# Kernel tuning notes

Hardware: AMD Instinct MI355X
Metric: run time of the kernel (lower is better)

The kernel has to match this reference:

```python
import jax, jax.numpy as jnp
import numpy as np

DIM = 1024
NH = 16        # query heads
NKV = 4        # kv heads
HD = 64        # head dim
GROUPS = NH // NKV
SPATIAL = 16
NZ = SPATIAL * SPATIAL  # 256 latent tokens with 2D structure
SOFT_CAP = 50.0
SCALE = HD ** -0.5
EPS = 1e-6


def rope_2d_cos_sin(nz, hd, spatial, dtype):
    # 2D RoPE: first half of head_dim encodes row position, second half column.
    pos = jnp.arange(nz)
    row = (pos // spatial).astype(jnp.float32)
    col = (pos % spatial).astype(jnp.float32)
    quarter = hd // 4
    inv_freq = 1.0 / (10000.0 ** (jnp.arange(quarter, dtype=jnp.float32) / quarter))
    f_row = row[:, None] * inv_freq[None, :]   # (nz, hd/4)
    f_col = col[:, None] * inv_freq[None, :]   # (nz, hd/4)
    emb = jnp.concatenate([f_row, f_col], axis=-1)      # (nz, hd/2)
    emb = jnp.concatenate([emb, emb], axis=-1)          # (nz, hd)
    return jnp.cos(emb).astype(dtype), jnp.sin(emb).astype(dtype)


def rotate_half(x):
    x1, x2 = jnp.split(x, 2, axis=-1)
    return jnp.concatenate([-x2, x1], axis=-1)


def apply_rotary(x, cos, sin):
    return x * cos + rotate_half(x) * sin


def rms_norm(x, w):
    # RMSNorm over head_dim with learned per-dim scale (QKNorm)
    return x * jax.lax.rsqrt(jnp.mean(x * x, axis=-1, keepdims=True) + EPS) * w


def setup_inputs() -> dict:
    key = jax.random.key(0)
    ks = jax.random.split(key, 7)
    B, T, S = 4, 16, 264
    x = jax.random.normal(ks[0], (B, T, S, DIM), dtype=jnp.float32)
    wq = jax.random.normal(ks[1], (NH * HD, DIM), dtype=jnp.float32) * 0.02
    wk = jax.random.normal(ks[2], (NKV * HD, DIM), dtype=jnp.float32) * 0.02
    wv = jax.random.normal(ks[3], (NKV * HD, DIM), dtype=jnp.float32) * 0.02
    wo = jax.random.normal(ks[4], (DIM, NH * HD), dtype=jnp.float32) * 0.02
    q_norm_w = jnp.ones((HD,), dtype=jnp.float32)
    k_norm_w = jnp.ones((HD,), dtype=jnp.float32)
    return {"x": x, "wq": wq, "wk": wk, "wv": wv, "wo": wo,
            "q_norm_w": q_norm_w, "k_norm_w": k_norm_w}


def reference(x, wq, wk, wv, wo, q_norm_w, k_norm_w):
    B, T, S, D = x.shape
    xf = x.reshape(B * T, S, D)
    # projections (torch Linear: y = x @ W.T)
    q = (xf @ wq.T).reshape(B * T, S, NH, HD).transpose(0, 2, 1, 3)   # (BT,NH,S,HD)
    k = (xf @ wk.T).reshape(B * T, S, NKV, HD).transpose(0, 2, 1, 3)  # (BT,NKV,S,HD)
    v = (xf @ wv.T).reshape(B * T, S, NKV, HD).transpose(0, 2, 1, 3)
    # QKNorm
    q = rms_norm(q, q_norm_w)
    k = rms_norm(k, k_norm_w)
    # partial 2D RoPE on latent tokens only
    cos, sin = rope_2d_cos_sin(NZ, HD, SPATIAL, q.dtype)
    cos = cos[None, None]  # (1,1,NZ,HD)
    sin = sin[None, None]
    q = jnp.concatenate([apply_rotary(q[:, :, :NZ], cos, sin), q[:, :, NZ:]], axis=2)
    k = jnp.concatenate([apply_rotary(k[:, :, :NZ], cos, sin), k[:, :, NZ:]], axis=2)
    # GQA: expand kv heads (repeat_interleave == jnp.repeat)
    k = jnp.repeat(k, GROUPS, axis=1)
    v = jnp.repeat(v, GROUPS, axis=1)
    # attention with soft cap
    attn = jnp.einsum("bhqd,bhkd->bhqk", q, k) * SCALE
    attn = SOFT_CAP * jnp.tanh(attn / SOFT_CAP)
    attn = jax.nn.softmax(attn, axis=-1)
    out = jnp.einsum("bhqk,bhkd->bhqd", attn, v)
    out = out.transpose(0, 2, 1, 3).reshape(B * T, S, NH * HD)
    out = out @ wo.T
    return out.reshape(B, T, S, D)
```

## Files before the change

kernel.cpp:

```cpp
#include <hip/hip_runtime.h>

typedef __bf16 bf16;
typedef __bf16 bf16x8 __attribute__((ext_vector_type(8)));
typedef float  f32x4  __attribute__((ext_vector_type(4)));
typedef float  f32x16 __attribute__((ext_vector_type(16)));
typedef unsigned int u32;

#define DIM   1024
#define NH    16
#define NKV   4
#define HD    64
#define SLEN  264
#define BTOT  64
#define MROWS (BTOT * SLEN)
#define NQKV  1536
#define NZ    256
#define VPAD  288

__device__ __forceinline__ void gl_lds16(const bf16* g, bf16* l) {
    __builtin_amdgcn_global_load_lds((__attribute__((address_space(1))) void*)(g),
                                     (__attribute__((address_space(3))) void*)(l),
                                     16, 0, 0);
}

__global__ void cvt_f32_bf16(const float* __restrict__ src, bf16* __restrict__ dst, int n) {
    int i = (blockIdx.x * 256 + threadIdx.x) * 4;
    if (i < n) {
        float4 v = *(const float4*)(src + i);
        dst[i + 0] = (bf16)v.x; dst[i + 1] = (bf16)v.y;
        dst[i + 2] = (bf16)v.z; dst[i + 3] = (bf16)v.w;
    }
}

__global__ void prep_misc(const float* __restrict__ wq, const float* __restrict__ wk,
                          const float* __restrict__ wv, const float* __restrict__ wo,
                          bf16* __restrict__ wcat, bf16* __restrict__ wobf,
                          float2* __restrict__ ctab) {
    int b = blockIdx.x, tid = threadIdx.x;
    if (b < 1536) {
        int i = (b * 256 + tid) * 4;
        const float* src; int off;
        if (i < 1024 * 1024)      { src = wq; off = i; }
        else if (i < 1280 * 1024) { src = wk; off = i - 1024 * 1024; }
        else                      { src = wv; off = i - 1280 * 1024; }
        float4 v = *(const float4*)(src + off);
        wcat[i + 0] = (bf16)v.x; wcat[i + 1] = (bf16)v.y;
        wcat[i + 2] = (bf16)v.z; wcat[i + 3] = (bf16)v.w;
    } else if (b < 2560) {
        int i = ((b - 1536) * 256 + tid) * 4;
        float4 v = *(const float4*)(wo + i);
        wobf[i + 0] = (bf16)v.x; wobf[i + 1] = (bf16)v.y;
        wobf[i + 2] = (bf16)v.z; wobf[i + 3] = (bf16)v.w;
    } else {
        int i = (b - 2560) * 256 + tid;
        int s = i >> 5, d = i & 31;
        const float LN1 = 0.5756462732485115f;
        float pos = (d < 16) ? (float)(s >> 4) : (float)(s & 15);
        float ang = pos * expf(-(float)(d & 15) * LN1);
        float sn, cs; sincosf(ang, &sn, &cs);
        ctab[i] = make_float2(cs, sn);
    }
}

__device__ __forceinline__ int xcd_swizzle(int orig, int nwg) {
    int q = nwg >> 3, r = nwg & 7;
    int xcd = orig & 7, lid = orig >> 3;
    return (xcd < r ? xcd * (q + 1) : r * (q + 1) + (xcd - r) * q) + lid;
}

#define GATE2  asm volatile("s_waitcnt vmcnt(2)" ::: "memory")
#define NOGATE do {} while (0)

#define STAGE(DST, G, H, KT) do {                                              \
    gl_lds16((G) + (size_t)((H) * 128 + rs0) * DIM + (KT) * 64 + cs0 * 8,      \
             (DST) + wid * 512);                                               \
    gl_lds16((G) + (size_t)((H) * 128 + 64 + rs0) * DIM + (KT) * 64 + cs0 * 8, \
             (DST) + 4096 + wid * 512);                                        \
} while (0)

#define PHASE(Ad, Bd, AA, KS, STAGE_STMT, GATE_STMT) do {                      \
    bf16x8 af_[4], bf_[4];                                                     \
    _Pragma("unroll")                                                          \
    for (int i_ = 0; i_ < 4; i_++) {                                           \
        af_[i_] = *(const bf16x8*)((Ad) + aRdBase + i_ * 1024 + xorv[KS]);     \
        bf_[i_] = *(const bf16x8*)((Bd) + bRdBase + i_ * 1024 + xorv[KS]);     \
    }                                                                          \
    STAGE_STMT;                                                                \
    GATE_STMT;                                                                 \
    __builtin_amdgcn_s_barrier();                                              \
    asm volatile("s_waitcnt lgkmcnt(0)" ::: "memory");                         \
    __builtin_amdgcn_sched_barrier(0);                                         \
    __builtin_amdgcn_s_setprio(1);                                             \
    _Pragma("unroll")                                                          \
    for (int i_ = 0; i_ < 4; i_++)                                             \
        _Pragma("unroll")                                                      \
        for (int n_ = 0; n_ < 4; n_++)                                         \
            acc[AA][i_][n_] = __builtin_amdgcn_mfma_f32_16x16x32_bf16(         \
                af_[i_], bf_[n_], acc[AA][i_][n_], 0, 0, 0);                   \
    __builtin_amdgcn_s_setprio(0);                                             \
    __builtin_amdgcn_s_barrier();                                              \
} while (0)

__device__ __forceinline__ void gemm256_core(const bf16* __restrict__ Ag,
                                             const bf16* __restrict__ Bg,
                                             f32x4 (&acc)[2][4][4]) {
    __shared__ __align__(16) bf16 A00[128 * 64], A01[128 * 64], A10[128 * 64], A11[128 * 64];
    __shared__ __align__(16) bf16 B00[128 * 64], B01[128 * 64], B10[128 * 64], B11[128 * 64];

    const int tid  = threadIdx.x;
    const int wid  = tid >> 6, lane = tid & 63;
    const int quad = lane >> 4, r16 = lane & 15;
    const int wm = wid & 1, wn = wid >> 1;

    const int rs0 = tid >> 3;
    const int cs0 = (tid & 7) ^ (rs0 & 7);

    const int aRdBase = (wm * 64 + r16) * 64;
    const int bRdBase = ((wn & 1) * 64 + r16) * 64;
    const int xorv[2] = { (quad ^ (r16 & 7)) * 8, ((4 + quad) ^ (r16 & 7)) * 8 };

    const bf16* Bd0 = (wn & 2) ? B01 : B00;
    const bf16* Bd1 = (wn & 2) ? B11 : B10;

    STAGE(A00, Ag, 0, 0);
    STAGE(A01, Ag, 1, 0);
    STAGE(B00, Bg, 0, 0);
    STAGE(B01, Bg, 1, 0);
    STAGE(A10, Ag, 0, 1);
    GATE2;
    __builtin_amdgcn_s_barrier();

#pragma unroll 1
    for (int it = 0; it < 8; ++it) {
        const int t1 = 2 * it + 1;
        int t2 = 2 * it + 2; if (t2 > 15) t2 = 15;
        int t3 = 2 * it + 3; if (t3 > 15) t3 = 15;
        PHASE(A00, Bd0, 0, 0, STAGE(A11, Ag, 1, t1), NOGATE);
        PHASE(A00, Bd0, 0, 1, STAGE(B10, Bg, 0, t1), NOGATE);
        PHASE(A01, Bd0, 1, 0, STAGE(B11, Bg, 1, t1), NOGATE);
        PHASE(A01, Bd0, 1, 1, STAGE(A00, Ag, 0, t2), GATE2);
        PHASE(A10, Bd1, 0, 0, STAGE(A01, Ag, 1, t2), NOGATE);
        PHASE(A10, Bd1, 0, 1, STAGE(B00, Bg, 0, t2), NOGATE);
        PHASE(A11, Bd1, 1, 0, STAGE(B01, Bg, 1, t2), NOGATE);
        PHASE(A11, Bd1, 1, 1, STAGE(A10, Ag, 0, t3), GATE2);
    }
}

__global__ __launch_bounds__(512) void gemm_qkv(const bf16* __restrict__ A,
                                                const bf16* __restrict__ Bw,
                                                bf16* __restrict__ out,
                                                const float* __restrict__ qw,
                                                const float* __restrict__ kw,
                                                const float2* __restrict__ ctab) {
    const int nwg = (MROWS / 256) * (NQKV / 256);
    int wg = xcd_swizzle(blockIdx.x, nwg);
    const int bm = wg / 6, bn = wg - bm * 6;

    f32x4 acc[2][4][4];
#pragma unroll
    for (int a = 0; a < 2; a++)
#pragma unroll
        for (int i = 0; i < 4; i++)
#pragma unroll
            for (int n = 0; n < 4; n++) acc[a][i][n] = (f32x4){0.f, 0.f, 0.f, 0.f};

    gemm256_core(A + (size_t)bm * 256 * DIM, Bw + (size_t)bn * 256 * DIM, acc);

    const int tid  = threadIdx.x;
    const int wid  = tid >> 6, lane = tid & 63;
    const int quad = lane >> 4, r16 = lane & 15;
    const int wm = wid & 1, wn = wid >> 1;
    const int colbase = bn * 256 + wn * 64;
    const int rowb    = bm * 256 + wm * 64;

    if (bn < 5) {
        const float* w = (bn < 4) ? qw : kw;
        float wreg[4];
#pragma unroll
        for (int n = 0; n < 4; n++) wreg[n] = w[n * 16 + r16];
#pragma unroll
        for (int a = 0; a < 2; a++)
#pragma unroll
            for (int i = 0; i < 4; i++)
#pragma unroll
                for (int r = 0; r < 4; r++) {
                    float ss = 0.f;
#pragma unroll
                    for (int n = 0; n < 4; n++) ss += acc[a][i][n][r] * acc[a][i][n][r];
                    ss += __shfl_xor(ss, 1, 64);
                    ss += __shfl_xor(ss, 2, 64);
                    ss += __shfl_xor(ss, 4, 64);
                    ss += __shfl_xor(ss, 8, 64);
                    float rms = rsqrtf(ss * (1.f / 64.f) + 1e-6f);
                    float xv[4];
#pragma unroll
                    for (int n = 0; n < 4; n++) xv[n] = acc[a][i][n][r] * rms * wreg[n];
                    int gm = rowb + a * 128 + i * 16 + quad * 4 + r;
                    int s = gm % SLEN;
                    if (s < NZ) {
                        float2 cs0 = ctab[s * 32 + r16];
                        float2 cs1 = ctab[s * 32 + 16 + r16];
                        float a0 = xv[0] * cs0.x - xv[2] * cs0.y;
                        float a2 = xv[2] * cs0.x + xv[0] * cs0.y;
                        float a1 = xv[1] * cs1.x - xv[3] * cs1.y;
                        float a3 = xv[3] * cs1.x + xv[1] * cs1.y;
                        xv[0] = a0; xv[1] = a1; xv[2] = a2; xv[3] = a3;
                    }
                    size_t rowoff = (size_t)gm * NQKV + colbase + r16;
#pragma unroll
                    for (int n = 0; n < 4; n++) out[rowoff + n * 16] = (bf16)xv[n];
                }
    } else {
#pragma unroll
        for (int a = 0; a < 2; a++)
#pragma unroll
            for (int i = 0; i < 4; i++)
#pragma unroll
                for (int r = 0; r < 4; r++) {
                    int gm = rowb + a * 128 + i * 16 + quad * 4 + r;
                    size_t rowoff = (size_t)gm * NQKV + colbase + r16;
#pragma unroll
                    for (int n = 0; n < 4; n++) out[rowoff + n * 16] = (bf16)acc[a][i][n][r];
                }
    }
}

#define GEMM_STAGE_PTRS(Mptr, tileRow, K, P)                                   \
    const bf16* P[4];                                                          \
    {                                                                          \
        _Pragma("unroll")                                                      \
        for (int k = 0; k < 4; k++) {                                          \
            int s = k * 256 + tid;                                             \
            int r = s >> 3, cp = s & 7;                                        \
            int c = cp ^ (r & 7);                                              \
            P[k] = (Mptr) + (size_t)((tileRow) + r) * (K) + c * 8;             \
        }                                                                      \
    }

__device__ __forceinline__ int swz(int row, int chunk) {
    return row * 64 + ((chunk ^ (row & 7)) * 8);
}

__global__ __launch_bounds__(256) void gemm_bt(const bf16* __restrict__ A,
                                               const bf16* __restrict__ Bw,
                                               float* __restrict__ Cout) {
    __shared__ __align__(16) bf16 As[128 * 64];
    __shared__ __align__(16) bf16 Bs[128 * 64];
    const int tid  = threadIdx.x;
    const int wid  = tid >> 6, lane = tid & 63;
    const int quad = lane >> 4, r16 = lane & 15;
    const int bid = blockIdx.x;
    const int g = bid / 32, rr = bid - g * 32;
    const int bm = g * 4 + (rr & 3), bn = rr >> 2;
    const int wm = wid & 1, wn = wid >> 1;

    GEMM_STAGE_PTRS(A,  bm * 128, DIM, Ap)
    GEMM_STAGE_PTRS(Bw, bn * 128, DIM, Bp)

    f32x4 acc[4][4];
#pragma unroll
    for (int i = 0; i < 4; i++)
#pragma unroll
        for (int j = 0; j < 4; j++) acc[i][j] = (f32x4){0.f, 0.f, 0.f, 0.f};

    for (int k0 = 0; k0 < DIM; k0 += 64) {
        __syncthreads();
#pragma unroll
        for (int k = 0; k < 4; k++) {
            gl_lds16(Ap[k] + k0, As + (k * 256 + wid * 64) * 8);
            gl_lds16(Bp[k] + k0, Bs + (k * 256 + wid * 64) * 8);
        }
        __syncthreads();
#pragma unroll
        for (int ks = 0; ks < 2; ks++) {
            bf16x8 a[4], b[4];
#pragma unroll
            for (int i = 0; i < 4; i++) {
                a[i] = *(const bf16x8*)&As[swz(wm * 64 + i * 16 + r16, ks * 4 + quad)];
                b[i] = *(const bf16x8*)&Bs[swz(wn * 64 + i * 16 + r16, ks * 4 + quad)];
            }
#pragma unroll
            for (int i = 0; i < 4; i++)
#pragma unroll
                for (int j = 0; j < 4; j++)
                    acc[i][j] = __builtin_amdgcn_mfma_f32_16x16x32_bf16(a[i], b[j], acc[i][j], 0, 0, 0);
        }
    }

#pragma unroll
    for (int i = 0; i < 4; i++)
#pragma unroll
        for (int j = 0; j < 4; j++)
#pragma unroll
            for (int r = 0; r < 4; r++) {
                int gm = bm * 128 + wm * 64 + i * 16 + quad * 4 + r;
                int gn = bn * 128 + wn * 64 + j * 16 + r16;
                Cout[(size_t)gm * DIM + gn] = acc[i][j][r];
            }
}

__global__ __launch_bounds__(256) void vtrans_kernel(const bf16* __restrict__ qkv,
                                                     bf16* __restrict__ vt) {
    __shared__ bf16 Ls[64 * 272];
    const int tid = threadIdx.x;
    const int b = blockIdx.x, bt = b >> 2, kv = b & 3;
    const int part = tid >> 5;
    const int rr   = tid & 31;
#pragma unroll
    for (int pass = 0; pass < 9; ++pass) {
        int row = pass * 32 + rr;
        if (row < SLEN) {
            bf16x8 v = *(const bf16x8*)(qkv + (size_t)(bt * SLEN + row) * NQKV + 1280 + kv * 64 + part * 8);
#pragma unroll
            for (int j = 0; j < 8; j++) Ls[(part * 8 + j) * 272 + row] = v[j];
        }
    }
    __syncthreads();
    const int d = tid >> 2, seg = tid & 3;
    size_t obase = ((size_t)b * 64 + d) * VPAD;
#pragma unroll
    for (int m = 0; m < 9; ++m) {
        int col = seg * 72 + m * 8;
        bf16x8 o;
#pragma unroll
        for (int j = 0; j < 8; j++) {
            int s = col + j;
            o[j] = (s < SLEN) ? Ls[d * 272 + s] : (bf16)0.f;
        }
        *(bf16x8*)(vt + obase + col) = o;
    }
}

__global__ __launch_bounds__(256) void attn_kernel(const bf16* __restrict__ qkv,
                                                   const bf16* __restrict__ vt,
                                                   bf16* __restrict__ aout) {
    __shared__ __align__(16) bf16 Kb[2][64 * 64];
    __shared__ __align__(16) bf16 Vb[2][64 * 64];
    __shared__ float invL[4][32];

    const int tid = threadIdx.x;
    const int wid = tid >> 6, lane = tid & 63;
    const int l31 = lane & 31, hi = lane >> 5;
    const int qp = blockIdx.x;
    const int kv = blockIdx.y, bt = blockIdx.z;
    const int h = kv * 4 + wid;

    int q0 = qp * 32 + l31;
    int qcl = q0 < SLEN ? q0 : SLEN - 1;
    const bf16* qbase = qkv + (size_t)(bt * SLEN + qcl) * NQKV + h * HD + hi * 8;
    bf16x8 qb[4];
#pragma unroll
    for (int s = 0; s < 4; s++) qb[s] = *(const bf16x8*)(qbase + s * 16);

    const int r0  = tid >> 3;
    const int r1  = r0 + 32;
    const int kc0 = (tid & 7) ^ (r0 & 7);
    const bf16* kg = qkv + (size_t)bt * SLEN * NQKV + 1024 + kv * 64 + kc0 * 8;
    const bf16* vg = vt + (size_t)(bt * 4 + kv) * HD * VPAD;

#define STAGEP(PB, P64) do {                                                     \
    int kr0 = (P64) + r0; if (kr0 > SLEN - 1) kr0 = SLEN - 1;                    \
    int kr1 = (P64) + r1; if (kr1 > SLEN - 1) kr1 = SLEN - 1;                    \
    gl_lds16(kg + (size_t)kr0 * NQKV, &Kb[PB][tid * 8]);                         \
    gl_lds16(kg + (size_t)kr1 * NQKV, &Kb[PB][(tid + 256) * 8]);                 \
    int vo = (P64) + kc0 * 8; if (vo > VPAD - 8) vo = VPAD - 8;                  \
    gl_lds16(vg + (size_t)r0 * VPAD + vo, &Vb[PB][tid * 8]);                     \
    gl_lds16(vg + (size_t)r1 * VPAD + vo, &Vb[PB][(tid + 256) * 8]);             \
} while (0)

    const int xorb = l31 & 7;
    int koff[4];
#pragma unroll
    for (int s = 0; s < 4; s++) koff[s] = l31 * 64 + (((s * 2 + hi) ^ xorb) * 8);

    f32x16 oacc[2];
#pragma unroll
    for (int r = 0; r < 16; r++) { oacc[0][r] = 0.f; oacc[1][r] = 0.f; }
    float lsum = 0.f;

    STAGEP(0, 0);
    __syncthreads();

#pragma unroll 1
    for (int p = 0; p < 5; ++p) {
        const int pb = p & 1;
        if (p < 4) STAGEP(pb ^ 1, (p + 1) * 64);
        const int hmax = (p == 4) ? 1 : 2;
        for (int hh = 0; hh < hmax; ++hh) {
            const bf16* Kp = &Kb[pb][hh * 2048];
            f32x16 sacc;
#pragma unroll
            for (int r = 0; r < 16; r++) sacc[r] = 0.f;
#pragma unroll
            for (int s = 0; s < 4; s++) {
                bf16x8 ka = *(const bf16x8*)(Kp + koff[s]);
                sacc = __builtin_amdgcn_mfma_f32_32x32x16_bf16(ka, qb[s], sacc, 0, 0, 0);
            }
            const int keyb = p * 64 + hh * 32;
            float pr[16];
#pragma unroll
            for (int r = 0; r < 16; ++r) {
                float sc = sacc[r];
                float t = sc * sc;
                float w = fmaf(t, 9.392546e-13f, -3.7570183e-7f);
                w = fmaf(t, w, 0.18033688f);
                float pv = exp2f(sc * w);
                int key = keyb + (r & 3) + 8 * (r >> 2) + 4 * hi;
                pv = (key < SLEN) ? pv : 0.f;
                pr[r] = pv;
                lsum += pv;
            }
#pragma unroll
            for (int st = 0; st < 2; st++) {
                u32 wA, wB, wC, wD;
                asm("v_cvt_pk_bf16_f32 %0, %1, %2" : "=v"(wA) : "v"(pr[st*8+0]), "v"(pr[st*8+1]));
                asm("v_cvt_pk_bf16_f32 %0, %1, %2" : "=v"(wB) : "v"(pr[st*8+2]), "v"(pr[st*8+3]));
                asm("v_cvt_pk_bf16_f32 %0, %1, %2" : "=v"(wC) : "v"(pr[st*8+4]), "v"(pr[st*8+5]));
                asm("v_cvt_pk_bf16_f32 %0, %1, %2" : "=v"(wD) : "v"(pr[st*8+6]), "v"(pr[st*8+7]));
                asm volatile("v_permlane32_swap_b32 %0, %1" : "+v"(wA), "+v"(wC));
                asm volatile("v_permlane32_swap_b32 %0, %1" : "+v"(wB), "+v"(wD));
                union { u32 u[4]; bf16x8 v; } pa;
                pa.u[0] = wA; pa.u[1] = wB; pa.u[2] = wC; pa.u[3] = wD;
#pragma unroll
                for (int dt = 0; dt < 2; dt++) {
                    bf16x8 vbf = *(const bf16x8*)(&Vb[pb][(dt * 32 + l31) * 64 +
                                         (((hh * 4 + st * 2 + hi) ^ xorb) * 8)]);
                    oacc[dt] = __builtin_amdgcn_mfma_f32_32x32x16_bf16(pa.v, vbf, oacc[dt], 0, 0, 0);
                }
            }
        }
        if (p < 4) __syncthreads();
    }
#undef STAGEP

    lsum += __shfl_xor(lsum, 32, 64);
    invL[wid][l31] = 1.f / lsum;
#pragma unroll
    for (int r = 0; r < 16; ++r) {
        int qloc = (r & 3) + 8 * (r >> 2) + 4 * hi;
        int q = qp * 32 + qloc;
        if (q < SLEN) {
            float inv = invL[wid][qloc];
            size_t base = (size_t)(bt * SLEN + q) * (NH * HD) + h * HD + l31;
            aout[base]      = (bf16)(oacc[0][r] * inv);
            aout[base + 32] = (bf16)(oacc[1][r] * inv);
        }
    }
}

extern "C" void kernel_launch(void* const* d_in, const int* in_sizes, int n_in,
                              void* d_out, int out_size, void* d_ws, size_t ws_size,
                              hipStream_t stream) {
    const float* x   = (const float*)d_in[0];
    const float* wq  = (const float*)d_in[1];
    const float* wk  = (const float*)d_in[2];
    const float* wv  = (const float*)d_in[3];
    const float* wo  = (const float*)d_in[4];
    const float* qnw = (const float*)d_in[5];
    const float* knw = (const float*)d_in[6];

    bf16* xbf  = (bf16*)d_ws;
    bf16* wcat = xbf  + (size_t)MROWS * DIM;
    bf16* wobf = wcat + (size_t)NQKV * DIM;
    bf16* qkv  = wobf + (size_t)DIM * DIM;
    bf16* vt   = qkv  + (size_t)MROWS * NQKV;
    float2* ctab = (float2*)(vt + (size_t)BTOT * NKV * HD * VPAD);
    bf16* aout = xbf;

    prep_misc<<<2592, 256, 0, stream>>>(wq, wk, wv, wo, wcat, wobf, ctab);
    cvt_f32_bf16<<<(MROWS * DIM) / 1024, 256, 0, stream>>>(x, xbf, MROWS * DIM);

    gemm_qkv<<<(MROWS / 256) * (NQKV / 256), 512, 0, stream>>>(xbf, wcat, qkv, qnw, knw, ctab);
    vtrans_kernel<<<BTOT * NKV, 256, 0, stream>>>(qkv, vt);
    attn_kernel<<<dim3(9, NKV, BTOT), 256, 0, stream>>>(qkv, vt, aout);
    gemm_bt<<<(MROWS / 128) * (DIM / 128), 256, 0, stream>>>(aout, wobf, (float*)d_out);
}
```

Measured before the change: 335.3 us.

## Fuse V transpose into QKV GEMM epilogue and merge input conversion into prep

The QKV GEMM epilogue for the V column block now writes V directly in transposed, padded layout into the vt buffer, using 4-wide bf16 stores. This removes the separate vtrans kernel and its read-back of V from the qkv buffer. The padding columns of vt are zeroed in the prep kernel, which now also absorbs the fp32-to-bf16 conversion of x, so one launch replaces two. The trade-off is that the V epilogue stores are strided by VPAD rows, so they coalesce less well than the previous row-major writes.

```diff
diff --git a/kernel.cpp b/kernel.cpp
--- a/kernel.cpp
+++ b/kernel.cpp
@@ -1,6 +1,7 @@
 #include <hip/hip_runtime.h>
 
 typedef __bf16 bf16;
+typedef __bf16 bf16x4 __attribute__((ext_vector_type(4)));
 typedef __bf16 bf16x8 __attribute__((ext_vector_type(8)));
 typedef float  f32x4  __attribute__((ext_vector_type(4)));
 typedef float  f32x16 __attribute__((ext_vector_type(16)));
@@ -23,22 +24,23 @@
                                      16, 0, 0);
 }
 
-__global__ void cvt_f32_bf16(const float* __restrict__ src, bf16* __restrict__ dst, int n) {
-    int i = (blockIdx.x * 256 + threadIdx.x) * 4;
-    if (i < n) {
-        float4 v = *(const float4*)(src + i);
-        dst[i + 0] = (bf16)v.x; dst[i + 1] = (bf16)v.y;
-        dst[i + 2] = (bf16)v.z; dst[i + 3] = (bf16)v.w;
-    }
-}
-
-__global__ void prep_misc(const float* __restrict__ wq, const float* __restrict__ wk,
+__global__ void prep_misc(const float* __restrict__ x,
+                          const float* __restrict__ wq, const float* __restrict__ wk,
                           const float* __restrict__ wv, const float* __restrict__ wo,
-                          bf16* __restrict__ wcat, bf16* __restrict__ wobf,
-                          float2* __restrict__ ctab) {
+                          bf16* __restrict__ xbf, bf16* __restrict__ wcat,
+                          bf16* __restrict__ wobf, float2* __restrict__ ctab,
+                          bf16* __restrict__ vt) {
     int b = blockIdx.x, tid = threadIdx.x;
-    if (b < 1536) {
+    if (b < 16896) {
         int i = (b * 256 + tid) * 4;
+        float4 v = *(const float4*)(x + i);
+        xbf[i + 0] = (bf16)v.x; xbf[i + 1] = (bf16)v.y;
+        xbf[i + 2] = (bf16)v.z; xbf[i + 3] = (bf16)v.w;
+        return;
+    }
+    int b2 = b - 16896;
+    if (b2 < 1536) {
+        int i = (b2 * 256 + tid) * 4;
         const float* src; int off;
         if (i < 1024 * 1024)      { src = wq; off = i; }
         else if (i < 1280 * 1024) { src = wk; off = i - 1024 * 1024; }
@@ -46,19 +48,24 @@
         float4 v = *(const float4*)(src + off);
         wcat[i + 0] = (bf16)v.x; wcat[i + 1] = (bf16)v.y;
         wcat[i + 2] = (bf16)v.z; wcat[i + 3] = (bf16)v.w;
-    } else if (b < 2560) {
-        int i = ((b - 1536) * 256 + tid) * 4;
+    } else if (b2 < 2560) {
+        int i = ((b2 - 1536) * 256 + tid) * 4;
         float4 v = *(const float4*)(wo + i);
         wobf[i + 0] = (bf16)v.x; wobf[i + 1] = (bf16)v.y;
         wobf[i + 2] = (bf16)v.z; wobf[i + 3] = (bf16)v.w;
-    } else {
-        int i = (b - 2560) * 256 + tid;
+    } else if (b2 < 2592) {
+        int i = (b2 - 2560) * 256 + tid;
         int s = i >> 5, d = i & 31;
         const float LN1 = 0.5756462732485115f;
         float pos = (d < 16) ? (float)(s >> 4) : (float)(s & 15);
         float ang = pos * expf(-(float)(d & 15) * LN1);
         float sn, cs; sincosf(ang, &sn, &cs);
         ctab[i] = make_float2(cs, sn);
+    } else {
+        int idx = (b2 - 2592) * 256 + tid;
+        int row = idx / 3, c = idx - row * 3;
+        bf16x8 z = {};
+        *(bf16x8*)(vt + (size_t)row * VPAD + 264 + c * 8) = z;
     }
 }
 
@@ -149,6 +156,7 @@
 __global__ __launch_bounds__(512) void gemm_qkv(const bf16* __restrict__ A,
                                                 const bf16* __restrict__ Bw,
                                                 bf16* __restrict__ out,
+                                                bf16* __restrict__ vt,
                                                 const float* __restrict__ qw,
                                                 const float* __restrict__ kw,
                                                 const float2* __restrict__ ctab) {
@@ -214,14 +222,21 @@
 #pragma unroll
         for (int a = 0; a < 2; a++)
 #pragma unroll
-            for (int i = 0; i < 4; i++)
-#pragma unroll
-                for (int r = 0; r < 4; r++) {
-                    int gm = rowb + a * 128 + i * 16 + quad * 4 + r;
-                    size_t rowoff = (size_t)gm * NQKV + colbase + r16;
-#pragma unroll
-                    for (int n = 0; n < 4; n++) out[rowoff + n * 16] = (bf16)acc[a][i][n][r];
+            for (int i = 0; i < 4; i++) {
+                int gm0 = rowb + a * 128 + i * 16 + quad * 4;
+                int btv = gm0 / SLEN;
+                int key0 = gm0 - btv * SLEN;
+                bf16* vbase = vt + (size_t)(btv * 4 + wn) * 64 * VPAD + key0;
+#pragma unroll
+                for (int n = 0; n < 4; n++) {
+                    bf16x4 v4;
+                    v4[0] = (bf16)acc[a][i][n][0];
+                    v4[1] = (bf16)acc[a][i][n][1];
+                    v4[2] = (bf16)acc[a][i][n][2];
+                    v4[3] = (bf16)acc[a][i][n][3];
+                    *(bf16x4*)(vbase + (size_t)(n * 16 + r16) * VPAD) = v4;
                 }
+            }
     }
 }
 
@@ -299,38 +314,6 @@
             }
 }
 
-__global__ __launch_bounds__(256) void vtrans_kernel(const bf16* __restrict__ qkv,
-                                                     bf16* __restrict__ vt) {
-    __shared__ bf16 Ls[64 * 272];
-    const int tid = threadIdx.x;
-    const int b = blockIdx.x, bt = b >> 2, kv = b & 3;
-    const int part = tid >> 5;
-    const int rr   = tid & 31;
-#pragma unroll
-    for (int pass = 0; pass < 9; ++pass) {
-        int row = pass * 32 + rr;
-        if (row < SLEN) {
-            bf16x8 v = *(const bf16x8*)(qkv + (size_t)(bt * SLEN + row) * NQKV + 1280 + kv * 64 + part * 8);
-#pragma unroll
-            for (int j = 0; j < 8; j++) Ls[(part * 8 + j) * 272 + row] = v[j];
-        }
-    }
-    __syncthreads();
-    const int d = tid >> 2, seg = tid & 3;
-    size_t obase = ((size_t)b * 64 + d) * VPAD;
-#pragma unroll
-    for (int m = 0; m < 9; ++m) {
-        int col = seg * 72 + m * 8;
-        bf16x8 o;
-#pragma unroll
-        for (int j = 0; j < 8; j++) {
-            int s = col + j;
-            o[j] = (s < SLEN) ? Ls[d * 272 + s] : (bf16)0.f;
-        }
-        *(bf16x8*)(vt + obase + col) = o;
-    }
-}
-
 __global__ __launch_bounds__(256) void attn_kernel(const bf16* __restrict__ qkv,
                                                    const bf16* __restrict__ vt,
                                                    bf16* __restrict__ aout) {
@@ -467,11 +450,10 @@
     float2* ctab = (float2*)(vt + (size_t)BTOT * NKV * HD * VPAD);
     bf16* aout = xbf;
 
-    prep_misc<<<2592, 256, 0, stream>>>(wq, wk, wv, wo, wcat, wobf, ctab);
-    cvt_f32_bf16<<<(MROWS * DIM) / 1024, 256, 0, stream>>>(x, xbf, MROWS * DIM);
-
-    gemm_qkv<<<(MROWS / 256) * (NQKV / 256), 512, 0, stream>>>(xbf, wcat, qkv, qnw, knw, ctab);
-    vtrans_kernel<<<BTOT * NKV, 256, 0, stream>>>(qkv, vt);
+    prep_misc<<<16896 + 1536 + 1024 + 32 + 192, 256, 0, stream>>>(
+        x, wq, wk, wv, wo, xbf, wcat, wobf, ctab, vt);
+
+    gemm_qkv<<<(MROWS / 256) * (NQKV / 256), 512, 0, stream>>>(xbf, wcat, qkv, vt, qnw, knw, ctab);
     attn_kernel<<<dim3(9, NKV, BTOT), 256, 0, stream>>>(qkv, vt, aout);
     gemm_bt<<<(MROWS / 128) * (DIM / 128), 256, 0, stream>>>(aout, wobf, (float*)d_out);
 }
```

New measurement: 322.9 us. 3.7% less time.
